# Optimization experiments

Measured on AMD Instinct MI355X. Metric: run time of the kernel, lower is better.

The kernel has to match this reference:

```python
import jax, jax.numpy as jnp
import numpy as np

EPS_NORM = 1e-12   # F.normalize eps (denominator clamp)
EPS_PD = 1e-6      # F.pairwise_distance eps (added to the difference)
MARGIN = 0.3

B, D = 8192, 512


def setup_inputs() -> dict:
    key = jax.random.key(0)
    x = jax.random.normal(key, (B, D * 2), dtype=jnp.float32).reshape(B, 2, D)
    return {"x": x}


def reference(x):
    # x: [B, 2, D]  (anchor, positive)
    a = x[:, 0, :]
    p = x[:, 1, :]
    a = a / jnp.maximum(jnp.linalg.norm(a, axis=1, keepdims=True), EPS_NORM)
    p = p / jnp.maximum(jnp.linalg.norm(p, axis=1, keepdims=True), EPS_NORM)
    b, d = a.shape

    # output[i, j] = -||a_i - p_j + EPS_PD||^2, expanded so the BxB matrix
    # comes from one GEMM instead of a [B, D, B] broadcasted difference.
    sa2 = jnp.sum(a * a, axis=1)               # [B]
    sp2 = jnp.sum(p * p, axis=1)               # [B]
    dot = a @ p.T                              # [B, B]
    sa = jnp.sum(a, axis=1)                    # [B]
    sp = jnp.sum(p, axis=1)                    # [B]
    d2 = (sa2[:, None] + sp2[None, :] - 2.0 * dot
          + 2.0 * EPS_PD * (sa[:, None] - sp[None, :]) + d * (EPS_PD * EPS_PD))
    sim = -d2                                  # [B, B] similarity (detached in torch)

    # mineHardNegative with hard_rank=0, hard_prob=1: top-1 of descending sort
    # after removing the self index -> argmax over the row with diag masked.
    sim = jnp.where(jnp.eye(b, dtype=bool), -jnp.inf, sim)
    negidx = jnp.argmax(sim, axis=1)           # [B] int
    n = p[negidx]                              # hard negatives, [B, D]

    pos_d = jnp.linalg.norm(a - p + EPS_PD, axis=1)
    neg_d = jnp.linalg.norm(a - n + EPS_PD, axis=1)
    nloss = jnp.mean(jax.nn.relu(pos_d ** 2 - neg_d ** 2 + MARGIN))
    return nloss
```

## Files before the change

kernel.cpp:

```cpp
#include <hip/hip_runtime.h>
#include <stdint.h>
#include <math.h>

#define Bn 8192
#define Dn 512
#define EPSN 1e-12f
#define EPSP 1e-6f
#define MARG 0.3f
#define QS 256.0f
#define ISQ (2.0f / 65536.0f)


#define TKB 64
#define NKT (Dn / TKB)

typedef int   int4v __attribute__((ext_vector_type(4)));
typedef float f32x4 __attribute__((ext_vector_type(4)));

__device__ __forceinline__ void async16(const void* g, void* l) {
    __builtin_amdgcn_global_load_lds(
        (const __attribute__((address_space(1))) void*)g,
        (__attribute__((address_space(3))) void*)l,
        16, 0, 0);
}

__device__ __forceinline__ unsigned key32(float s) {
    union { float f; unsigned u; } c; c.f = s;
    return (c.u & 0x80000000u) ? ~c.u : (c.u | 0x80000000u);
}
__device__ __forceinline__ float unkey32(unsigned k) {
    union { unsigned u; float f; } c;
    c.u = (k & 0x80000000u) ? (k ^ 0x80000000u) : ~k;
    return c.f;
}

__global__ __launch_bounds__(256) void k_normalize(
    const float* __restrict__ x,
    uint8_t* __restrict__ a_i8, uint8_t* __restrict__ p_i8,
    float* __restrict__ cterm, float* __restrict__ rowconst,
    unsigned* __restrict__ rowmax)
{
    const int wave = threadIdx.x >> 6;
    const int lane = threadIdx.x & 63;
    const int i = blockIdx.x * 4 + wave;

    const float* srcA = x + (size_t)i * (2 * Dn) + lane * 8;
    const float* srcP = srcA + Dn;
    float4 a0 = ((const float4*)srcA)[0];
    float4 a1 = ((const float4*)srcA)[1];
    float4 p0 = ((const float4*)srcP)[0];
    float4 p1 = ((const float4*)srcP)[1];
    float va[8] = {a0.x, a0.y, a0.z, a0.w, a1.x, a1.y, a1.z, a1.w};
    float vp[8] = {p0.x, p0.y, p0.z, p0.w, p1.x, p1.y, p1.z, p1.w};

    float ssa = 0.f, ssp = 0.f;
#pragma unroll
    for (int j = 0; j < 8; ++j) { ssa += va[j] * va[j]; ssp += vp[j] * vp[j]; }
#pragma unroll
    for (int m = 1; m < 64; m <<= 1) {
        ssa += __shfl_xor(ssa, m);
        ssp += __shfl_xor(ssp, m);
    }
    const float sa = 1.0f / fmaxf(sqrtf(ssa), EPSN);
    const float sp = 1.0f / fmaxf(sqrtf(ssp), EPSN);

    float oa[8], op[8];
    float s1p = 0.f, s2p = 0.f, s1a = 0.f, s2a = 0.f, pos = 0.f;
#pragma unroll
    for (int j = 0; j < 8; ++j) {
        oa[j] = va[j] * sa;
        op[j] = vp[j] * sp;
        s1p += op[j]; s2p += op[j] * op[j];
        s1a += oa[j]; s2a += oa[j] * oa[j];
        const float u = oa[j] - op[j] + EPSP;
        pos += u * u;
    }

    uint64_t pka = 0, pkp = 0;
#pragma unroll
    for (int j = 0; j < 8; ++j) {
        int qa = (int)rintf(oa[j] * QS);
        int qp = (int)rintf(op[j] * QS);
        qa = qa > 127 ? 127 : (qa < -127 ? -127 : qa);
        qp = qp > 127 ? 127 : (qp < -127 ? -127 : qp);
        pka |= (uint64_t)(uint8_t)qa << (8 * j);
        pkp |= (uint64_t)(uint8_t)qp << (8 * j);
    }
    *(uint64_t*)(a_i8 + (size_t)i * Dn + lane * 8) = pka;
    *(uint64_t*)(p_i8 + (size_t)i * Dn + lane * 8) = pkp;

#pragma unroll
    for (int m = 1; m < 64; m <<= 1) {
        s1p += __shfl_xor(s1p, m);
        s2p += __shfl_xor(s2p, m);
        s1a += __shfl_xor(s1a, m);
        s2a += __shfl_xor(s2a, m);
        pos += __shfl_xor(pos, m);
    }
    if (lane == 0) {
        cterm[i] = -s2p + 2.0f * EPSP * s1p;
        rowconst[i] = pos - s2a - 2.0f * EPSP * s1a
                      - (float)Dn * EPSP * EPSP + MARG;
        rowmax[i] = 0u;
    }
}

__global__ __launch_bounds__(512, 2) void k_gemm_argmax(
    const uint8_t* __restrict__ a_i8, const uint8_t* __restrict__ p_i8,
    const float* __restrict__ cterm,
    unsigned* __restrict__ rowmax)
{
    __shared__ __align__(16) uint8_t As[4][256 * TKB];
    __shared__ __align__(16) uint8_t Bs[4][256 * TKB];
    __shared__ unsigned smx[2][256];

    const int t = threadIdx.x;
    const int wave = t >> 6;
    const int lane = t & 63;
    const int q = lane >> 4;
    const int m16 = lane & 15;
    const int wr = wave >> 2;
    const int wc = wave & 3;
    const int j0 = blockIdx.y * 256;
    const int i0 = blockIdx.x * 256;

    const int rr = t >> 2;
    const int gg = ((t & 3) ^ ((t >> 3) & 3)) * 16;
    const uint8_t* gA0 = p_i8 + (size_t)(j0 + rr) * Dn + gg;
    const uint8_t* gA1 = p_i8 + (size_t)(j0 + 128 + rr) * Dn + gg;
    const uint8_t* gB0 = a_i8 + (size_t)(i0 + rr) * Dn + gg;
    const uint8_t* gB1 = a_i8 + (size_t)(i0 + 128 + rr) * Dn + gg;
    const int ldsOff = wave * 1024;

    const int sl = (q ^ ((m16 >> 1) & 3)) * 16;
    const int aOff = (wr * 128 + m16) * TKB + sl;
    const int bOff = (wc * 64 + m16) * TKB + sl;

    auto stage1 = [&](int slot, int kb, int h) {
        switch (h) {
        case 0: async16(gA0 + kb, &As[slot][ldsOff]);        break;
        case 1: async16(gA1 + kb, &As[slot][8192 + ldsOff]); break;
        case 2: async16(gB0 + kb, &Bs[slot][ldsOff]);        break;
        case 3: async16(gB1 + kb, &Bs[slot][8192 + ldsOff]); break;
        }
    };

    int4v acc[8][4];
#pragma unroll
    for (int a = 0; a < 8; ++a)
#pragma unroll
        for (int b = 0; b < 4; ++b) acc[a][b] = (int4v){0, 0, 0, 0};

#pragma unroll
    for (int h = 0; h < 4; ++h) stage1(0, 0, h);
#pragma unroll
    for (int h = 0; h < 4; ++h) stage1(1, TKB, h);
    asm volatile("s_waitcnt vmcnt(4)" ::: "memory");
    __builtin_amdgcn_s_barrier();

#pragma unroll
    for (int kt = 0; kt < NKT; ++kt) {
        const int slot = kt & 3;
        const uint8_t* pa = &As[slot][aOff];
        const uint8_t* pb = &Bs[slot][bOff];

        int4v af[8], bf[4];
#pragma unroll
        for (int mt = 0; mt < 8; ++mt)
            af[mt] = *(const int4v*)(pa + mt * 1024);
#pragma unroll
        for (int nt = 0; nt < 4; ++nt)
            bf[nt] = *(const int4v*)(pb + nt * 1024);
        if (kt + 2 < NKT) {
#pragma unroll
            for (int h = 0; h < 4; ++h) stage1((kt + 2) & 3, (kt + 2) * TKB, h);
        }

        asm volatile("s_waitcnt lgkmcnt(0)" ::: "memory");
        __builtin_amdgcn_sched_barrier(0);
        __builtin_amdgcn_s_setprio(1);
#pragma unroll
        for (int mt = 0; mt < 8; ++mt)
#pragma unroll
            for (int nt = 0; nt < 4; ++nt)
                acc[mt][nt] = __builtin_amdgcn_mfma_i32_16x16x64_i8(
                    af[mt], bf[nt], acc[mt][nt], 0, 0, 0);
        __builtin_amdgcn_s_setprio(0);

        if (kt + 2 < NKT)
            asm volatile("s_waitcnt vmcnt(4)" ::: "memory");
        else if (kt + 2 == NKT)
            asm volatile("s_waitcnt vmcnt(0)" ::: "memory");
        if (kt + 1 < NKT) __builtin_amdgcn_s_barrier();
    }

    f32x4 cj[8];
#pragma unroll
    for (int mt = 0; mt < 8; ++mt)
        cj[mt] = *(const f32x4*)(cterm + j0 + wr * 128 + mt * 16 + q * 4);

    unsigned kv[4];
    const bool diag = (i0 == j0);
    if (!diag) {
#pragma unroll
        for (int nt = 0; nt < 4; ++nt) {
            float mx = -3.4e38f;
#pragma unroll
            for (int mt = 0; mt < 8; ++mt)
#pragma unroll
                for (int v = 0; v < 4; ++v)
                    mx = fmaxf(mx, ISQ * (float)acc[mt][nt][v] + cj[mt][v]);
            kv[nt] = key32(mx);
        }
    } else {
#pragma unroll
        for (int nt = 0; nt < 4; ++nt) {
            const int dtarget = wc * 64 + nt * 16 + m16 - wr * 128 - q * 4;
            float mx = -3.4e38f;
#pragma unroll
            for (int mt = 0; mt < 8; ++mt)
#pragma unroll
                for (int v = 0; v < 4; ++v) {
                    const float sc = ISQ * (float)acc[mt][nt][v] + cj[mt][v];
                    mx = (mt * 16 + v == dtarget) ? mx : fmaxf(mx, sc);
                }
            kv[nt] = key32(mx);
        }
    }

#pragma unroll
    for (int nt = 0; nt < 4; ++nt) {
#pragma unroll
        for (int msk = 16; msk < 64; msk <<= 1) {
            const unsigned o = (unsigned)__shfl_xor((int)kv[nt], msk);
            kv[nt] = o > kv[nt] ? o : kv[nt];
        }
    }
    if (lane < 16) {
#pragma unroll
        for (int nt = 0; nt < 4; ++nt)
            smx[wr][wc * 64 + nt * 16 + m16] = kv[nt];
    }
    __syncthreads();
    if (t < 256) {
        const unsigned k0 = smx[0][t];
        const unsigned k1 = smx[1][t];
        atomicMax(&rowmax[i0 + t], k0 > k1 ? k0 : k1);
    }
}

__global__ __launch_bounds__(1024) void k_final(
    const unsigned* __restrict__ rowmax,
    const float* __restrict__ rowconst,
    float* __restrict__ out)
{
    __shared__ float smf[16];
    float s = 0.f;
    for (int k = threadIdx.x; k < Bn; k += 1024)
        s += fmaxf(rowconst[k] + unkey32(rowmax[k]), 0.f);
#pragma unroll
    for (int msk = 1; msk < 64; msk <<= 1) s += __shfl_xor(s, msk);
    if ((threadIdx.x & 63) == 0) smf[threadIdx.x >> 6] = s;
    __syncthreads();
    if (threadIdx.x == 0) {
        float tot = 0.f;
#pragma unroll
        for (int w = 0; w < 16; ++w) tot += smf[w];
        out[0] = tot * (1.0f / Bn);
    }
}

extern "C" void kernel_launch(void* const* d_in, const int* in_sizes, int n_in,
                              void* d_out, int out_size, void* d_ws, size_t ws_size,
                              hipStream_t stream)
{
    const float* x = (const float*)d_in[0];
    char* ws = (char*)d_ws;
    uint8_t*  a_i8     = (uint8_t*)(ws + 0);
    uint8_t*  p_i8     = (uint8_t*)(ws + 4194304);
    float*    cterm    = (float*)(ws + 8388608);
    float*    rowconst = (float*)(ws + 8421376);
    unsigned* rowmax   = (unsigned*)(ws + 8454144);
    float*    out      = (float*)d_out;

    k_normalize<<<2048, 256, 0, stream>>>(x, a_i8, p_i8, cterm, rowconst, rowmax);
    k_gemm_argmax<<<dim3(Bn / 256, Bn / 256), 512, 0, stream>>>(
        a_i8, p_i8, cterm, rowmax);
    k_final<<<1, 1024, 0, stream>>>(rowmax, rowconst, out);
}
```

Measured before the change: 115.0 us.

## Double-buffer LDS fragment reads and deepen global prefetch to three tiles

Manually unrolls the int8 GEMM K-loop so each step loads the next tile's A/B fragments from LDS into a second register set while MFMAs run on the current set. Global-to-LDS staging now runs three tiles ahead instead of two, with the wait counts adjusted to match. The aim is to hide LDS read latency and global load latency behind MFMA work. In exchange it uses about 48 more VGPRs for the second fragment set, which could reduce occupancy or cause spills under the 512-thread, 2-block launch bounds.

```diff
diff --git a/kernel.cpp b/kernel.cpp
--- a/kernel.cpp
+++ b/kernel.cpp
@@ -105,6 +105,53 @@
     }
 }
 
+#define READ_FRAGS(AF, BF, SLOT)                                             \
+  {                                                                          \
+    const uint8_t* pa_ = &As[(SLOT)][aOff];                                  \
+    const uint8_t* pb_ = &Bs[(SLOT)][bOff];                                  \
+    BF[0] = *(const int4v*)(pb_ + 0 * 1024);                                 \
+    BF[1] = *(const int4v*)(pb_ + 1 * 1024);                                 \
+    BF[2] = *(const int4v*)(pb_ + 2 * 1024);                                 \
+    BF[3] = *(const int4v*)(pb_ + 3 * 1024);                                 \
+    AF[0] = *(const int4v*)(pa_ + 0 * 1024);                                 \
+    AF[1] = *(const int4v*)(pa_ + 1 * 1024);                                 \
+    AF[2] = *(const int4v*)(pa_ + 2 * 1024);                                 \
+    AF[3] = *(const int4v*)(pa_ + 3 * 1024);                                 \
+    AF[4] = *(const int4v*)(pa_ + 4 * 1024);                                 \
+    AF[5] = *(const int4v*)(pa_ + 5 * 1024);                                 \
+    AF[6] = *(const int4v*)(pa_ + 6 * 1024);                                 \
+    AF[7] = *(const int4v*)(pa_ + 7 * 1024);                                 \
+  }
+
+#define TILE_BODY(CAF, CBF, NAF, NBF, KT)                                    \
+  {                                                                          \
+    asm volatile("s_waitcnt lgkmcnt(0)" ::: "memory");                       \
+    __builtin_amdgcn_sched_barrier(0);     \
+    if ((KT) + 1 < NKT) READ_FRAGS(NAF, NBF, ((KT) + 1) & 3);                \
+    __builtin_amdgcn_sched_barrier(0);         \
+    if ((KT) + 3 < NKT) {                                                    \
+      stage1(((KT) + 3) & 3, ((KT) + 3) * TKB, 0);                           \
+      stage1(((KT) + 3) & 3, ((KT) + 3) * TKB, 1);                           \
+      stage1(((KT) + 3) & 3, ((KT) + 3) * TKB, 2);                           \
+      stage1(((KT) + 3) & 3, ((KT) + 3) * TKB, 3);                           \
+    }                                                                        \
+    __builtin_amdgcn_sched_barrier(0);                                       \
+    __builtin_amdgcn_s_setprio(1);                                           \
+    _Pragma("unroll")                                                        \
+    for (int mt_ = 0; mt_ < 8; ++mt_) {                                      \
+      _Pragma("unroll")                                                      \
+      for (int nt_ = 0; nt_ < 4; ++nt_)                                      \
+        acc[mt_][nt_] = __builtin_amdgcn_mfma_i32_16x16x64_i8(               \
+            CAF[mt_], CBF[nt_], acc[mt_][nt_], 0, 0, 0);                     \
+    }                                                                        \
+    __builtin_amdgcn_s_setprio(0);                                           \
+    if ((KT) + 3 < NKT)                                                      \
+      asm volatile("s_waitcnt vmcnt(4)" ::: "memory");                       \
+    else if ((KT) + 3 == NKT)                                                \
+      asm volatile("s_waitcnt vmcnt(0)" ::: "memory");                       \
+    if ((KT) + 1 < NKT) __builtin_amdgcn_s_barrier();                        \
+  }
+
 __global__ __launch_bounds__(512, 2) void k_gemm_argmax(
     const uint8_t* __restrict__ a_i8, const uint8_t* __restrict__ p_i8,
     const float* __restrict__ cterm,
@@ -151,48 +198,27 @@
 #pragma unroll
         for (int b = 0; b < 4; ++b) acc[a][b] = (int4v){0, 0, 0, 0};
 
+    int4v afA[8], bfA[4], afB[8], bfB[4];
+
 #pragma unroll
     for (int h = 0; h < 4; ++h) stage1(0, 0, h);
 #pragma unroll
     for (int h = 0; h < 4; ++h) stage1(1, TKB, h);
+#pragma unroll
+    for (int h = 0; h < 4; ++h) stage1(2, 2 * TKB, h);
     asm volatile("s_waitcnt vmcnt(4)" ::: "memory");
     __builtin_amdgcn_s_barrier();
-
-#pragma unroll
-    for (int kt = 0; kt < NKT; ++kt) {
-        const int slot = kt & 3;
-        const uint8_t* pa = &As[slot][aOff];
-        const uint8_t* pb = &Bs[slot][bOff];
-
-        int4v af[8], bf[4];
-#pragma unroll
-        for (int mt = 0; mt < 8; ++mt)
-            af[mt] = *(const int4v*)(pa + mt * 1024);
-#pragma unroll
-        for (int nt = 0; nt < 4; ++nt)
-            bf[nt] = *(const int4v*)(pb + nt * 1024);
-        if (kt + 2 < NKT) {
-#pragma unroll
-            for (int h = 0; h < 4; ++h) stage1((kt + 2) & 3, (kt + 2) * TKB, h);
-        }
-
-        asm volatile("s_waitcnt lgkmcnt(0)" ::: "memory");
-        __builtin_amdgcn_sched_barrier(0);
-        __builtin_amdgcn_s_setprio(1);
-#pragma unroll
-        for (int mt = 0; mt < 8; ++mt)
-#pragma unroll
-            for (int nt = 0; nt < 4; ++nt)
-                acc[mt][nt] = __builtin_amdgcn_mfma_i32_16x16x64_i8(
-                    af[mt], bf[nt], acc[mt][nt], 0, 0, 0);
-        __builtin_amdgcn_s_setprio(0);
-
-        if (kt + 2 < NKT)
-            asm volatile("s_waitcnt vmcnt(4)" ::: "memory");
-        else if (kt + 2 == NKT)
-            asm volatile("s_waitcnt vmcnt(0)" ::: "memory");
-        if (kt + 1 < NKT) __builtin_amdgcn_s_barrier();
-    }
+    READ_FRAGS(afA, bfA, 0);
+    __builtin_amdgcn_sched_barrier(0);
+
+    TILE_BODY(afA, bfA, afB, bfB, 0)
+    TILE_BODY(afB, bfB, afA, bfA, 1)
+    TILE_BODY(afA, bfA, afB, bfB, 2)
+    TILE_BODY(afB, bfB, afA, bfA, 3)
+    TILE_BODY(afA, bfA, afB, bfB, 4)
+    TILE_BODY(afB, bfB, afA, bfA, 5)
+    TILE_BODY(afA, bfA, afB, bfB, 6)
+    TILE_BODY(afB, bfB, afA, bfA, 7)
 
     f32x4 cj[8];
 #pragma unroll
```

Result: no change. 114.6 us (-0.4%).
